# Performance work log

Measured on AMD Instinct MI355X. Metric: run time of the kernel, lower is better.

The kernel has to match this reference:

```python
import jax, jax.numpy as jnp
import numpy as np

B, L, E, H, DV, V = 256, 512, 200, 256, 30000, 50000
NEG_INF = -jnp.inf

def setup_inputs() -> dict:
    key = jax.random.key(0)
    ks = jax.random.split(key, 16)
    s = 0.05
    f = jnp.float32
    return {
        "input_id": jax.random.randint(ks[0], (B, 1), 0, V),
        "input_emb": jax.random.normal(ks[1], (B, 1, E), f),
        "encoder_outputs": jax.random.normal(ks[2], (B, L, H), f),
        "encoder_input_ids": jax.random.randint(ks[3], (B, L), 0, V),
        "hidden": jax.random.normal(ks[4], (B, 1, H), f),
        "attention": jax.random.normal(ks[5], (B, 1, H), f),
        # GRU (PyTorch layout): W_ih (3H, 2H+E), W_hh (3H, H), gate order r,z,n
        "W_ih": jax.random.normal(ks[6], (3 * H, 2 * H + E), f) * s,
        "W_hh": jax.random.normal(ks[7], (3 * H, H), f) * s,
        "b_ih": jnp.zeros((3 * H,), f),
        "b_hh": jnp.zeros((3 * H,), f),
        "W_attn": jax.random.normal(ks[8], (H, H), f) * s,
        "b_attn": jnp.zeros((H,), f),
        "W_comb": jax.random.normal(ks[9], (H, 2 * H), f) * s,
        "b_comb": jnp.zeros((H,), f),
        "W_gen": jax.random.normal(ks[10], (DV, H), f) * s,
        "b_gen": jnp.zeros((DV,), f),
        "W_copy": jax.random.normal(ks[11], (H, H), f) * s,
        "b_copy": jnp.zeros((H,), f),
    }


def reference(input_id, input_emb, encoder_outputs, encoder_input_ids, hidden,
              attention, W_ih, W_hh, b_ih, b_hh, W_attn, b_attn, W_comb,
              b_comb, W_gen, b_gen, W_copy, b_copy):
    b, l = encoder_input_ids.shape
    # selective read: rou = normalized match mask (NaN guard -> 0)
    mask = (input_id == encoder_input_ids).astype(encoder_outputs.dtype)  # (b,l)
    msum = jnp.sum(mask, axis=1, keepdims=True)
    rou = jnp.where(msum > 0, mask / jnp.where(msum > 0, msum, 1.0), 0.0)
    selective_read = jnp.einsum('bl,blh->bh', rou, encoder_outputs)  # (b,h)

    # GRU single step (dropout is identity at inference)
    x = jnp.concatenate([input_emb[:, 0], attention[:, 0], selective_read], axis=-1)
    h_prev = hidden[:, 0]  # (b,h)
    gx = x @ W_ih.T + b_ih          # (b,3h)
    gh = h_prev @ W_hh.T + b_hh     # (b,3h)
    xr, xz, xn = jnp.split(gx, 3, axis=-1)
    hr, hz, hn = jnp.split(gh, 3, axis=-1)
    r = jax.nn.sigmoid(xr + hr)
    z = jax.nn.sigmoid(xz + hz)
    n = jnp.tanh(xn + r * hn)
    h = (1.0 - z) * n + z * h_prev  # (b,h) cur_hidden

    # attention
    q = h @ W_attn.T + b_attn
    attn_w = jax.nn.softmax(jnp.einsum('bh,blh->bl', q, encoder_outputs), axis=-1)
    attn_applied = jnp.einsum('bl,blh->bh', attn_w, encoder_outputs)
    cur_attention = jnp.tanh(
        jnp.concatenate([attn_applied, h], axis=-1) @ W_comb.T + b_comb)  # (b,h)

    # generate + copy scores, joint softmax
    generate_score = cur_attention @ W_gen.T + b_gen                     # (b,DV)
    copy_weights = jax.nn.sigmoid(encoder_outputs @ W_copy.T + b_copy)   # (b,l,h)
    copy_score = jnp.einsum('blh,bh->bl', copy_weights, cur_attention)   # (b,l)
    score = jax.nn.softmax(jnp.concatenate([generate_score, copy_score], axis=1), axis=1)
    gen_s, copy_s = score[:, :DV], score[:, DV:]

    # fused equivalent of the one-hot scatter/mix: direct scatter-add into vocab
    output = jnp.zeros((b, V), score.dtype)
    output = output.at[:, :DV].add(gen_s)
    output = output.at[jnp.arange(b)[:, None], encoder_input_ids].add(copy_s)

    pos = output > 0
    out = jnp.where(pos, jnp.log(jnp.where(pos, output, 1.0)), NEG_INF)
    return out, h[:, None, :], cur_attention[:, None, :]
```

## Files before the change

### kernel.cpp

```cpp
#include <hip/hip_runtime.h>
#include <cmath>

#define B_  256
#define L_  512
#define E_  200
#define H_  256
#define DV_ 30000
#define V_  50000
#define X_  712
#define G3_ 768
#define NT_ 235

#define NEG_BIG -1.0e30f

typedef __attribute__((ext_vector_type(8))) _Float16 half8;
typedef __attribute__((ext_vector_type(4))) float   floatx4;

#define GLOAD16(gptr, lptr)                                                            \
    __builtin_amdgcn_global_load_lds(                                                  \
        (const __attribute__((address_space(1))) unsigned int*)(gptr),                 \
        (__attribute__((address_space(3))) unsigned int*)(lptr), 16, 0, 0)

__global__ void k_selread(const int* __restrict__ input_id, const float* __restrict__ emb,
                          const float* __restrict__ attention, const float* __restrict__ hidden,
                          const float* __restrict__ enc, const int* __restrict__ enc_ids,
                          const float* __restrict__ Wc, _Float16* __restrict__ wcb,
                          float* __restrict__ xT) {
    int b = blockIdx.x, t = threadIdx.x;
    __shared__ int cnt;
    __shared__ int list[L_];
    if (t == 0) cnt = 0;
    __syncthreads();
    wcb[b * H_ + t] = (_Float16)Wc[b * H_ + t];
    int id = input_id[b];
    for (int l = t; l < L_; l += 256) {
        if (enc_ids[b * L_ + l] == id) { int p = atomicAdd(&cnt, 1); list[p] = l; }
    }
    __syncthreads();
    int n = cnt;
    float s = 0.f;
    for (int i = 0; i < n; i++) s += enc[(b * L_ + list[i]) * H_ + t];
    float sel = (n > 0) ? s / (float)n : 0.f;
    for (int k = t; k < E_; k += 256) xT[k * B_ + b] = emb[b * E_ + k];
    xT[(E_ + t) * B_ + b]       = attention[b * H_ + t];
    xT[(E_ + H_ + t) * B_ + b]  = sel;
    xT[(X_ + t) * B_ + b]       = hidden[b * H_ + t];
}

template<int K, int OS>
__global__ void __launch_bounds__(256) k_gru_one(const float* __restrict__ xTp, const float* __restrict__ W,
                                                 const float* __restrict__ bias, float* __restrict__ g) {
    __shared__ __align__(16) float Ws[8 * K];
    int t  = threadIdx.x;
    int j0 = blockIdx.x * 8;
    int bq = t & 63;
    int jh = t >> 6;
#pragma unroll
    for (int jj = 0; jj < 8; jj++) {
        const float4* src = (const float4*)(W + (size_t)(j0 + jj) * K);
        float4* dst = (float4*)(Ws + jj * K);
        for (int i = t; i < K / 4; i += 256) dst[i] = src[i];
    }
    __syncthreads();
    float acc0[4] = {0.f, 0.f, 0.f, 0.f};
    float acc1[4] = {0.f, 0.f, 0.f, 0.f};
    const float* w0 = Ws + (jh * 2 + 0) * K;
    const float* w1 = Ws + (jh * 2 + 1) * K;
#pragma unroll 2
    for (int k4 = 0; k4 < K / 4; k4++) {
        float4 wa = *(const float4*)(w0 + k4 * 4);
        float4 wb = *(const float4*)(w1 + k4 * 4);
        float wav[4] = {wa.x, wa.y, wa.z, wa.w};
        float wbv[4] = {wb.x, wb.y, wb.z, wb.w};
#pragma unroll
        for (int u = 0; u < 4; u++) {
            float4 xv = *(const float4*)(xTp + (size_t)(k4 * 4 + u) * B_ + bq * 4);
            acc0[0] += wav[u] * xv.x; acc0[1] += wav[u] * xv.y;
            acc0[2] += wav[u] * xv.z; acc0[3] += wav[u] * xv.w;
            acc1[0] += wbv[u] * xv.x; acc1[1] += wbv[u] * xv.y;
            acc1[2] += wbv[u] * xv.z; acc1[3] += wbv[u] * xv.w;
        }
    }
    int ja = j0 + jh * 2, jb = ja + 1;
    float ba = bias[ja], bb = bias[jb];
#pragma unroll
    for (int i = 0; i < 4; i++) {
        g[(size_t)(bq * 4 + i) * OS + ja] = acc0[i] + ba;
        g[(size_t)(bq * 4 + i) * OS + jb] = acc1[i] + bb;
    }
}

__global__ void k_gru_gates(const float* __restrict__ gx, const float* __restrict__ gh,
                            const float* __restrict__ hidden, float* __restrict__ hws,
                            float* __restrict__ hT, float* __restrict__ hout) {
    int b = blockIdx.x, j = threadIdx.x;
    float xr = gx[b * G3_ + j], xz = gx[b * G3_ + 256 + j], xn = gx[b * G3_ + 512 + j];
    float hr = gh[b * G3_ + j], hz = gh[b * G3_ + 256 + j], hn = gh[b * G3_ + 512 + j];
    float r = 1.f / (1.f + expf(-(xr + hr)));
    float z = 1.f / (1.f + expf(-(xz + hz)));
    float n = tanhf(xn + r * hn);
    float hp = hidden[b * H_ + j];
    float h = (1.f - z) * n + z * hp;
    hws[b * H_ + j] = h;
    hT[j * B_ + b]  = h;
    hout[b * H_ + j] = h;
}

#define NC_ 4
#define CR_ 128
__global__ void __launch_bounds__(256) k_attn_a(const float* __restrict__ qws, const float* __restrict__ enc,
                         float* __restrict__ avp, float* __restrict__ mdp) {
    int blk = blockIdx.x;
    int b = blk >> 2, c = blk & 3;
    int t = threadIdx.x, lane = t & 63, w = t >> 6;
    __shared__ float ps[CR_];
    __shared__ float red[8];
    __shared__ __align__(16) float pavs[4][H_];
    const float* encc = enc + ((size_t)b * L_ + c * CR_) * H_;
    float4 q4 = *(const float4*)&qws[b * H_ + lane * 4];
    for (int i = 0; i < 32; i += 8) {
        float s[8];
#pragma unroll
        for (int u = 0; u < 8; u++) {
            float4 e = *(const float4*)(encc + (size_t)(w * 32 + i + u) * H_ + lane * 4);
            s[u] = q4.x * e.x + q4.y * e.y + q4.z * e.z + q4.w * e.w;
        }
#pragma unroll
        for (int u = 0; u < 8; u++) {
#pragma unroll
            for (int o = 1; o < 64; o <<= 1) s[u] += __shfl_xor(s[u], o);
            if (lane == 0) ps[w * 32 + i + u] = s[u];
        }
    }
    __syncthreads();
    {
        float v = ps[w * 32 + (lane & 31)];
#pragma unroll
        for (int o = 1; o < 64; o <<= 1) v = fmaxf(v, __shfl_xor(v, o));
        if (lane == 0) red[w] = v;
    }
    __syncthreads();
    float M = fmaxf(fmaxf(red[0], red[1]), fmaxf(red[2], red[3]));
    float e = (t < CR_) ? __expf(ps[t] - M) : 0.f;
    {
        float ssum = e;
#pragma unroll
        for (int o = 1; o < 64; o <<= 1) ssum += __shfl_xor(ssum, o);
        if (lane == 0) red[4 + w] = ssum;
    }
    __syncthreads();
    if (t < CR_) ps[t] = e;
    if (t == 0) {
        mdp[blk * 2]     = M;
        mdp[blk * 2 + 1] = red[4] + red[5] + red[6] + red[7];
    }
    __syncthreads();
    {
        float4 av = {0.f, 0.f, 0.f, 0.f};
        const float* encg = encc + (size_t)w * 32 * H_;
        const float* psg  = &ps[w * 32];
#pragma unroll 4
        for (int r = 0; r < 32; r++) {
            float p = psg[r];
            float4 ev = *(const float4*)(encg + (size_t)r * H_ + lane * 4);
            av.x += p * ev.x; av.y += p * ev.y; av.z += p * ev.z; av.w += p * ev.w;
        }
        *(float4*)&pavs[w][lane * 4] = av;
    }
    __syncthreads();
    avp[(size_t)blk * H_ + t] = pavs[0][t] + pavs[1][t] + pavs[2][t] + pavs[3][t];
}

__global__ void __launch_bounds__(256) k_attn_b(const float* __restrict__ avp, const float* __restrict__ mdp,
                         const float* __restrict__ hws, const float* __restrict__ W_comb,
                         const float* __restrict__ b_comb,
                         float* __restrict__ caws, _Float16* __restrict__ cab,
                         float* __restrict__ caout) {
    int b = blockIdx.x, t = threadIdx.x;
    __shared__ __align__(16) float xs[2 * H_];
    float m0 = mdp[(b * 4 + 0) * 2], d0 = mdp[(b * 4 + 0) * 2 + 1];
    float m1 = mdp[(b * 4 + 1) * 2], d1 = mdp[(b * 4 + 1) * 2 + 1];
    float m2 = mdp[(b * 4 + 2) * 2], d2 = mdp[(b * 4 + 2) * 2 + 1];
    float m3 = mdp[(b * 4 + 3) * 2], d3 = mdp[(b * 4 + 3) * 2 + 1];
    float M = fmaxf(fmaxf(m0, m1), fmaxf(m2, m3));
    float f0 = __expf(m0 - M), f1 = __expf(m1 - M), f2 = __expf(m2 - M), f3 = __expf(m3 - M);
    float den = f0 * d0 + f1 * d1 + f2 * d2 + f3 * d3;
    float num = f0 * avp[((size_t)b * 4 + 0) * H_ + t] + f1 * avp[((size_t)b * 4 + 1) * H_ + t]
              + f2 * avp[((size_t)b * 4 + 2) * H_ + t] + f3 * avp[((size_t)b * 4 + 3) * H_ + t];
    xs[t]      = num / den;
    xs[H_ + t] = hws[b * H_ + t];
    __syncthreads();
    const float4* wr = (const float4*)(W_comb + (size_t)t * (2 * H_));
    const float4* xp = (const float4*)xs;
    float acc = 0.f;
#pragma unroll 8
    for (int k4 = 0; k4 < 128; k4++) {
        float4 wv = wr[k4], xv = xp[k4];
        acc += wv.x * xv.x + wv.y * xv.y + wv.z * xv.z + wv.w * xv.w;
    }
    float cav = tanhf(b_comb[t] + acc);
    caws[b * H_ + t]  = cav;
    cab[b * H_ + t]   = (_Float16)cav;
    caout[b * H_ + t] = cav;
}

__global__ void __launch_bounds__(256, 2) k_gen_mfma(
        const _Float16* __restrict__ cab, const float* __restrict__ W_gen,
        const float* __restrict__ b_gen, float* __restrict__ out,
        float2* __restrict__ pmd) {
    __shared__ __align__(16) _Float16 Ah[128 * 32];
    __shared__ __align__(16) float    Bf[128 * 32];
    __shared__ float mm[4][128], dd[4][128];
    int t = threadIdx.x, w = t >> 6, lane = t & 63;
    int n0 = blockIdx.x * 128, m0 = blockIdx.y * 128;
    int wm = (w >> 1) * 64, wn = (w & 1) * 64;
    int l15 = lane & 15, q = lane >> 4;
    floatx4 acc[4][4];
#pragma unroll
    for (int i = 0; i < 4; i++)
#pragma unroll
        for (int j = 0; j < 4; j++) acc[i][j] = (floatx4){0.f, 0.f, 0.f, 0.f};

    for (int kc = 0; kc < H_; kc += 32) {
#pragma unroll
        for (int i = 0; i < 2; i++) {
            int t2 = w * 2 + i;
            int row = t2 * 16 + (lane >> 2);
            int sl  = (lane & 3) ^ ((row >> 1) & 3);
            const _Float16* g = cab + (size_t)(m0 + row) * H_ + kc + sl * 8;
            GLOAD16(g, &Ah[t2 * 512]);
        }
#pragma unroll
        for (int i = 0; i < 4; i++) {
            int t2 = w * 4 + i;
            int row = t2 * 8 + (lane >> 3);
            int sl  = (lane & 7) ^ (row & 7);
            int nn = n0 + row; nn = nn < DV_ ? nn : DV_ - 1;
            const float* g = W_gen + (size_t)nn * H_ + kc + sl * 4;
            GLOAD16(g, &Bf[t2 * 256]);
        }
        __syncthreads();
        half8 a[4];
#pragma unroll
        for (int mi = 0; mi < 4; mi++) {
            int m = wm + mi * 16 + l15;
            a[mi] = *(const half8*)&Ah[m * 32 + (q ^ ((m >> 1) & 3)) * 8];
        }
#pragma unroll
        for (int ni = 0; ni < 4; ni++) {
            int n = wn + ni * 16 + l15;
            const float* bb = &Bf[n * 32];
            float4 f0 = *(const float4*)&bb[((q * 2 + 0) ^ (n & 7)) * 4];
            float4 f1 = *(const float4*)&bb[((q * 2 + 1) ^ (n & 7)) * 4];
            half8 bf;
            bf[0] = (_Float16)f0.x; bf[1] = (_Float16)f0.y; bf[2] = (_Float16)f0.z; bf[3] = (_Float16)f0.w;
            bf[4] = (_Float16)f1.x; bf[5] = (_Float16)f1.y; bf[6] = (_Float16)f1.z; bf[7] = (_Float16)f1.w;
#pragma unroll
            for (int mi = 0; mi < 4; mi++)
                acc[mi][ni] = __builtin_amdgcn_mfma_f32_16x16x32_f16(a[mi], bf, acc[mi][ni], 0, 0, 0);
        }
        __syncthreads();
    }
    float bgs[4];
#pragma unroll
    for (int ni = 0; ni < 4; ni++) {
        int col = n0 + wn + ni * 16 + l15;
        if (col < DV_) {
            float bg = b_gen[col];
            bgs[ni] = bg;
#pragma unroll
            for (int mi = 0; mi < 4; mi++)
#pragma unroll
                for (int j = 0; j < 4; j++) {
                    int row = m0 + wm + mi * 16 + q * 4 + j;
                    out[(size_t)row * V_ + col] = acc[mi][ni][j] + bg;
                }
        } else bgs[ni] = 0.f;
    }
#pragma unroll
    for (int mi = 0; mi < 4; mi++)
#pragma unroll
        for (int j = 0; j < 4; j++) {
            float m_l = -INFINITY, d_l = 0.f;
#pragma unroll
            for (int ni = 0; ni < 4; ni++) {
                int col = n0 + wn + ni * 16 + l15;
                float v = (col < DV_) ? acc[mi][ni][j] + bgs[ni] : NEG_BIG;
                float mn = fmaxf(m_l, v);
                d_l = d_l * __expf(m_l - mn) + __expf(v - mn);
                m_l = mn;
            }
#pragma unroll
            for (int o = 1; o < 16; o <<= 1) {
                float m2 = __shfl_xor(m_l, o), d2 = __shfl_xor(d_l, o);
                float mn = fmaxf(m_l, m2);
                d_l = d_l * __expf(m_l - mn) + d2 * __expf(m2 - mn);
                m_l = mn;
            }
            if (l15 == 0) {
                int rl = wm + mi * 16 + q * 4 + j;
                mm[w][rl] = m_l; dd[w][rl] = d_l;
            }
        }
    __syncthreads();
    if (t < 128) {
        int wa = (t < 64) ? 0 : 2;
        float ma = mm[wa][t],     da = dd[wa][t];
        float mb = mm[wa + 1][t], db = dd[wa + 1][t];
        float M = fmaxf(ma, mb);
        float D = da * __expf(ma - M) + db * __expf(mb - M);
        pmd[(size_t)(m0 + t) * NT_ + blockIdx.x] = make_float2(M, D);
    }
}

__global__ void __launch_bounds__(256, 2) k_copy_mfma(
        const float* __restrict__ enc, const _Float16* __restrict__ wcb,
        const float* __restrict__ b_copy, const float* __restrict__ caws,
        float* __restrict__ copy_s) {
    __shared__ __align__(16) float    Af[128 * 32];
    __shared__ __align__(16) _Float16 Bh[256 * 32];
    __shared__ float bcs[H_], cas[H_];
    int t = threadIdx.x, w = t >> 6, lane = t & 63;
    int R0 = blockIdx.x * 128;
    int b  = blockIdx.x >> 2;
    int l15 = lane & 15, q = lane >> 4;
    bcs[t] = b_copy[t];
    cas[t] = caws[b * H_ + t];
    floatx4 acc[2][16];
#pragma unroll
    for (int i = 0; i < 2; i++)
#pragma unroll
        for (int j = 0; j < 16; j++) acc[i][j] = (floatx4){0.f, 0.f, 0.f, 0.f};

    for (int kc = 0; kc < H_; kc += 32) {
#pragma unroll
        for (int i = 0; i < 4; i++) {
            int t2 = w * 4 + i;
            int row = t2 * 8 + (lane >> 3);
            int sl  = (lane & 7) ^ (row & 7);
            const float* g = enc + (size_t)(R0 + row) * H_ + kc + sl * 4;
            GLOAD16(g, &Af[t2 * 256]);
        }
#pragma unroll
        for (int i = 0; i < 4; i++) {
            int t2 = w * 4 + i;
            int row = t2 * 16 + (lane >> 2);
            int sl  = (lane & 3) ^ ((row >> 1) & 3);
            const _Float16* g = wcb + row * H_ + kc + sl * 8;
            GLOAD16(g, &Bh[t2 * 512]);
        }
        __syncthreads();
        half8 a[2];
#pragma unroll
        for (int mi = 0; mi < 2; mi++) {
            int m = w * 32 + mi * 16 + l15;
            const float* ar = &Af[m * 32];
            float4 f0 = *(const float4*)&ar[((q * 2 + 0) ^ (m & 7)) * 4];
            float4 f1 = *(const float4*)&ar[((q * 2 + 1) ^ (m & 7)) * 4];
            half8 h;
            h[0] = (_Float16)f0.x; h[1] = (_Float16)f0.y; h[2] = (_Float16)f0.z; h[3] = (_Float16)f0.w;
            h[4] = (_Float16)f1.x; h[5] = (_Float16)f1.y; h[6] = (_Float16)f1.z; h[7] = (_Float16)f1.w;
            a[mi] = h;
        }
#pragma unroll
        for (int ni = 0; ni < 16; ni++) {
            int n = ni * 16 + l15;
            half8 bf = *(const half8*)&Bh[n * 32 + (q ^ ((n >> 1) & 3)) * 8];
            acc[0][ni] = __builtin_amdgcn_mfma_f32_16x16x32_f16(a[0], bf, acc[0][ni], 0, 0, 0);
            acc[1][ni] = __builtin_amdgcn_mfma_f32_16x16x32_f16(a[1], bf, acc[1][ni], 0, 0, 0);
        }
        __syncthreads();
    }
#pragma unroll
    for (int mi = 0; mi < 2; mi++) {
#pragma unroll
        for (int j = 0; j < 4; j++) {
            float p = 0.f;
#pragma unroll
            for (int ni = 0; ni < 16; ni++) {
                int col = ni * 16 + l15;
                float v = acc[mi][ni][j] + bcs[col];
                p += cas[col] / (1.f + __expf(-v));
            }
            p += __shfl_xor(p, 1);
            p += __shfl_xor(p, 2);
            p += __shfl_xor(p, 4);
            p += __shfl_xor(p, 8);
            if (l15 == 0) copy_s[R0 + w * 32 + mi * 16 + q * 4 + j] = p;
        }
    }
}

__global__ void __launch_bounds__(256) k_stats2(const float2* __restrict__ pmd, const float* __restrict__ copy_s,
                         float* __restrict__ mrow, float* __restrict__ ldrow) {
    int b = blockIdx.x, t = threadIdx.x, lane = t & 63, w = t >> 6;
    __shared__ float rm[4], rs[4];
    float m = -INFINITY, d = 0.f;
    if (t < NT_) { float2 p = pmd[(size_t)b * NT_ + t]; m = p.x; d = p.y; }
    float v0 = copy_s[b * L_ + t];
    float v1 = copy_s[b * L_ + 256 + t];
    float mn = fmaxf(m, v0); d = d * __expf(m - mn) + __expf(v0 - mn); m = mn;
    mn = fmaxf(m, v1); d = d * __expf(m - mn) + __expf(v1 - mn); m = mn;
#pragma unroll
    for (int o = 1; o < 64; o <<= 1) {
        float m2 = __shfl_xor(m, o), d2 = __shfl_xor(d, o);
        mn = fmaxf(m, m2);
        d = d * __expf(m - mn) + d2 * __expf(m2 - mn);
        m = mn;
    }
    if (lane == 0) { rm[w] = m; rs[w] = d; }
    __syncthreads();
    if (t == 0) {
        float M = rm[0], S = rs[0];
        for (int i = 1; i < 4; i++) {
            float mx = fmaxf(M, rm[i]);
            S = S * __expf(M - mx) + rs[i] * __expf(rm[i] - mx);
            M = mx;
        }
        mrow[b] = M;
        ldrow[b] = __logf(S);
    }
}

__global__ void __launch_bounds__(256) k_final(float* __restrict__ out, const float* __restrict__ mrow,
                        const float* __restrict__ ldrow) {
    int idx = blockIdx.x * 256 + threadIdx.x;
    int b = blockIdx.y;
    if (idx >= V_ / 4) return;
    float4* o4 = (float4*)(out + (size_t)b * V_) + idx;
    if (idx >= DV_ / 4) {
        *o4 = make_float4(NEG_BIG, NEG_BIG, NEG_BIG, NEG_BIG);
        return;
    }
    float sh = mrow[b] + ldrow[b];
    float4 v = *o4;
    v.x -= sh; v.y -= sh; v.z -= sh; v.w -= sh;
    *o4 = v;
}

__global__ void k_scatter_log(float* __restrict__ out, const float* __restrict__ copy_s,
                              const int* __restrict__ enc_ids, const float* __restrict__ mrow,
                              const float* __restrict__ ldrow) {
    int l = blockIdx.x * 256 + threadIdx.x;
    int b = blockIdx.y;
    float p = __expf(copy_s[b * L_ + l] - mrow[b] - ldrow[b]);
    unsigned int* up = (unsigned int*)(out + (size_t)b * V_ + enc_ids[b * L_ + l]);
    unsigned int cur = *up;
    while (true) {
        float ov = __uint_as_float(cur);
        float pv = (ov < -1.0e29f) ? p : __expf(ov) + p;
        unsigned int prev = atomicCAS(up, cur, __float_as_uint(__logf(pv)));
        if (prev == cur) break;
        cur = prev;
    }
}

extern "C" void kernel_launch(void* const* d_in, const int* in_sizes, int n_in,
                              void* d_out, int out_size, void* d_ws, size_t ws_size,
                              hipStream_t stream) {
    const int*   input_id  = (const int*)  d_in[0];
    const float* input_emb = (const float*)d_in[1];
    const float* enc       = (const float*)d_in[2];
    const int*   enc_ids   = (const int*)  d_in[3];
    const float* hidden    = (const float*)d_in[4];
    const float* attention = (const float*)d_in[5];
    const float* W_ih      = (const float*)d_in[6];
    const float* W_hh      = (const float*)d_in[7];
    const float* b_ih      = (const float*)d_in[8];
    const float* b_hh      = (const float*)d_in[9];
    const float* W_attn    = (const float*)d_in[10];
    const float* b_attn    = (const float*)d_in[11];
    const float* W_comb    = (const float*)d_in[12];
    const float* b_comb    = (const float*)d_in[13];
    const float* W_gen     = (const float*)d_in[14];
    const float* b_gen     = (const float*)d_in[15];
    const float* W_copy    = (const float*)d_in[16];
    const float* b_copy    = (const float*)d_in[17];

    float* out = (float*)d_out;
    float* ws  = (float*)d_ws;
    float* xT   = ws;
    float* gx   = xT + 247808;
    float* gh   = gx + 196608;
    float* hws  = gh + 196608;
    float* caws = hws + 65536;
    float* cps  = caws + 65536;
    float* mrow = cps + 131072;
    float* ldrow = mrow + 256;
    _Float16* wcb = (_Float16*)(ldrow + 256);
    _Float16* cab = wcb + 65536;
    float* qws  = (float*)(cab + 65536);
    float* mdp  = qws + 65536;
    float2* pmd = (float2*)(mdp + 2048);
    float* hT   = xT;
    float* avp  = gx;

    float* hout  = out + (size_t)B_ * V_;
    float* caout = hout + B_ * H_;

    k_selread<<<256, 256, 0, stream>>>(input_id, input_emb, attention, hidden, enc, enc_ids, W_copy, wcb, xT);
    k_gru_one<712, G3_><<<96, 256, 0, stream>>>(xT, W_ih, b_ih, gx);
    k_gru_one<256, G3_><<<96, 256, 0, stream>>>(xT + X_ * B_, W_hh, b_hh, gh);
    k_gru_gates<<<256, 256, 0, stream>>>(gx, gh, hidden, hws, hT, hout);
    k_gru_one<256, H_><<<32, 256, 0, stream>>>(hT, W_attn, b_attn, qws);
    k_attn_a<<<B_ * NC_, 256, 0, stream>>>(qws, enc, avp, mdp);
    k_attn_b<<<256, 256, 0, stream>>>(avp, mdp, hws, W_comb, b_comb, caws, cab, caout);
    k_gen_mfma<<<dim3(NT_, 2), 256, 0, stream>>>(cab, W_gen, b_gen, out, pmd);
    k_copy_mfma<<<(B_ * L_) / 128, 256, 0, stream>>>(enc, wcb, b_copy, caws, cps);
    k_stats2<<<256, 256, 0, stream>>>(pmd, cps, mrow, ldrow);
    dim3 gf((V_ / 4 + 255) / 256, B_);
    k_final<<<gf, 256, 0, stream>>>(out, mrow, ldrow);
    dim3 gs(L_ / 256, B_);
    k_scatter_log<<<gs, 256, 0, stream>>>(out, cps, enc_ids, mrow, ldrow);
}
```

Baseline: 447.6 us.

## Merge generate and copy GEMMs into one launch with double-buffered LDS staging

```diff
diff --git a/kernel.cpp b/kernel.cpp
--- a/kernel.cpp
+++ b/kernel.cpp
@@ -10,6 +10,8 @@
 #define X_  712
 #define G3_ 768
 #define NT_ 235
+#define NBC_ 1024
+#define NBG_ 470
 
 #define NEG_BIG -1.0e30f
 
@@ -204,189 +206,209 @@
     caout[b * H_ + t] = cav;
 }
 
-__global__ void __launch_bounds__(256, 2) k_gen_mfma(
+__global__ void __launch_bounds__(256, 2) k_gc(
+        const float* __restrict__ enc, const _Float16* __restrict__ wcb,
+        const float* __restrict__ b_copy, const float* __restrict__ caws,
+        float* __restrict__ copy_s,
         const _Float16* __restrict__ cab, const float* __restrict__ W_gen,
         const float* __restrict__ b_gen, float* __restrict__ out,
         float2* __restrict__ pmd) {
-    __shared__ __align__(16) _Float16 Ah[128 * 32];
-    __shared__ __align__(16) float    Bf[128 * 32];
-    __shared__ float mm[4][128], dd[4][128];
+    __shared__ __align__(16) unsigned char smem[67584];
     int t = threadIdx.x, w = t >> 6, lane = t & 63;
-    int n0 = blockIdx.x * 128, m0 = blockIdx.y * 128;
-    int wm = (w >> 1) * 64, wn = (w & 1) * 64;
     int l15 = lane & 15, q = lane >> 4;
-    floatx4 acc[4][4];
-#pragma unroll
-    for (int i = 0; i < 4; i++)
-#pragma unroll
-        for (int j = 0; j < 4; j++) acc[i][j] = (floatx4){0.f, 0.f, 0.f, 0.f};
-
-    for (int kc = 0; kc < H_; kc += 32) {
-#pragma unroll
-        for (int i = 0; i < 2; i++) {
-            int t2 = w * 2 + i;
-            int row = t2 * 16 + (lane >> 2);
-            int sl  = (lane & 3) ^ ((row >> 1) & 3);
-            const _Float16* g = cab + (size_t)(m0 + row) * H_ + kc + sl * 8;
-            GLOAD16(g, &Ah[t2 * 512]);
-        }
-#pragma unroll
-        for (int i = 0; i < 4; i++) {
-            int t2 = w * 4 + i;
-            int row = t2 * 8 + (lane >> 3);
-            int sl  = (lane & 7) ^ (row & 7);
-            int nn = n0 + row; nn = nn < DV_ ? nn : DV_ - 1;
-            const float* g = W_gen + (size_t)nn * H_ + kc + sl * 4;
-            GLOAD16(g, &Bf[t2 * 256]);
-        }
+
+    if (blockIdx.x < NBC_) {
+        float*    Af = (float*)smem;
+        _Float16* Bh = (_Float16*)(smem + 32768);
+        float*    bcs = (float*)(smem + 65536);
+        float*    cas = bcs + H_;
+        int cb = blockIdx.x;
+        int R0 = cb * 128;
+        int b  = cb >> 2;
+        bcs[t] = b_copy[t];
+        cas[t] = caws[b * H_ + t];
+        floatx4 acc[2][16];
+#pragma unroll
+        for (int i = 0; i < 2; i++)
+#pragma unroll
+            for (int j = 0; j < 16; j++) acc[i][j] = (floatx4){0.f, 0.f, 0.f, 0.f};
+
+#define STAGE_CPY(KC, BUF)                                                              \
+        {                                                                               \
+            _Pragma("unroll")                                                           \
+            for (int i = 0; i < 4; i++) {                                               \
+                int t2 = w * 4 + i;                                                     \
+                int row = t2 * 8 + (lane >> 3);                                         \
+                int sl  = (lane & 7) ^ (row & 7);                                       \
+                GLOAD16(enc + (size_t)(R0 + row) * H_ + (KC) + sl * 4,                  \
+                        &Af[(BUF) * 4096 + t2 * 256]);                                  \
+            }                                                                           \
+            _Pragma("unroll")                                                           \
+            for (int i = 0; i < 4; i++) {                                               \
+                int t2 = w * 4 + i;                                                     \
+                int row = t2 * 16 + (lane >> 2);                                        \
+                int sl  = (lane & 3) ^ ((row >> 1) & 3);                                \
+                GLOAD16(wcb + row * H_ + (KC) + sl * 8,                                 \
+                        &Bh[(BUF) * 8192 + t2 * 512]);                                  \
+            }                                                                           \
+        }
+        STAGE_CPY(0, 0);
         __syncthreads();
-        half8 a[4];
-#pragma unroll
-        for (int mi = 0; mi < 4; mi++) {
-            int m = wm + mi * 16 + l15;
-            a[mi] = *(const half8*)&Ah[m * 32 + (q ^ ((m >> 1) & 3)) * 8];
-        }
+        int cur = 0;
+        for (int kc8 = 0; kc8 < 8; kc8++) {
+            if (kc8 < 7) STAGE_CPY((kc8 + 1) * 32, cur ^ 1);
+            half8 a[2];
+#pragma unroll
+            for (int mi = 0; mi < 2; mi++) {
+                int m = w * 32 + mi * 16 + l15;
+                const float* ar = &Af[cur * 4096 + m * 32];
+                float4 f0 = *(const float4*)&ar[((q * 2 + 0) ^ (m & 7)) * 4];
+                float4 f1 = *(const float4*)&ar[((q * 2 + 1) ^ (m & 7)) * 4];
+                half8 h;
+                h[0] = (_Float16)f0.x; h[1] = (_Float16)f0.y; h[2] = (_Float16)f0.z; h[3] = (_Float16)f0.w;
+                h[4] = (_Float16)f1.x; h[5] = (_Float16)f1.y; h[6] = (_Float16)f1.z; h[7] = (_Float16)f1.w;
+                a[mi] = h;
+            }
+#pragma unroll
+            for (int ni = 0; ni < 16; ni++) {
+                int n = ni * 16 + l15;
+                half8 bf = *(const half8*)&Bh[cur * 8192 + n * 32 + (q ^ ((n >> 1) & 3)) * 8];
+                acc[0][ni] = __builtin_amdgcn_mfma_f32_16x16x32_f16(a[0], bf, acc[0][ni], 0, 0, 0);
+                acc[1][ni] = __builtin_amdgcn_mfma_f32_16x16x32_f16(a[1], bf, acc[1][ni], 0, 0, 0);
+            }
+            __syncthreads();
+            cur ^= 1;
+        }
+#pragma unroll
+        for (int mi = 0; mi < 2; mi++) {
+#pragma unroll
+            for (int j = 0; j < 4; j++) {
+                float p = 0.f;
+#pragma unroll
+                for (int ni = 0; ni < 16; ni++) {
+                    int col = ni * 16 + l15;
+                    float v = acc[mi][ni][j] + bcs[col];
+                    p += cas[col] / (1.f + __expf(-v));
+                }
+                p += __shfl_xor(p, 1);
+                p += __shfl_xor(p, 2);
+                p += __shfl_xor(p, 4);
+                p += __shfl_xor(p, 8);
+                if (l15 == 0) copy_s[R0 + w * 32 + mi * 16 + q * 4 + j] = p;
+            }
+        }
+    } else {
+        _Float16* Ah = (_Float16*)smem;
+        float*    Bf = (float*)(smem + 16384);
+        float*    mm = (float*)(smem + 49152);
+        float*    dd = mm + 512;
+        int g  = blockIdx.x - NBC_;
+        int bx = (g < NT_) ? g : g - NT_;
+        int by = (g < NT_) ? 0 : 1;
+        int n0 = bx * 128, m0 = by * 128;
+        int wm = (w >> 1) * 64, wn = (w & 1) * 64;
+        floatx4 acc[4][4];
+#pragma unroll
+        for (int i = 0; i < 4; i++)
+#pragma unroll
+            for (int j = 0; j < 4; j++) acc[i][j] = (floatx4){0.f, 0.f, 0.f, 0.f};
+
+#define STAGE_GEN(KC, BUF)                                                              \
+        {                                                                               \
+            _Pragma("unroll")                                                           \
+            for (int i = 0; i < 2; i++) {                                               \
+                int t2 = w * 2 + i;                                                     \
+                int row = t2 * 16 + (lane >> 2);                                        \
+                int sl  = (lane & 3) ^ ((row >> 1) & 3);                                \
+                GLOAD16(cab + (size_t)(m0 + row) * H_ + (KC) + sl * 8,                  \
+                        &Ah[(BUF) * 4096 + t2 * 512]);                                  \
+            }                                                                           \
+            _Pragma("unroll")                                                           \
+            for (int i = 0; i < 4; i++) {                                               \
+                int t2 = w * 4 + i;                                                     \
+                int row = t2 * 8 + (lane >> 3);                                         \
+                int sl  = (lane & 7) ^ (row & 7);                                       \
+                int nn = n0 + row; nn = nn < DV_ ? nn : DV_ - 1;                        \
+                GLOAD16(W_gen + (size_t)nn * H_ + (KC) + sl * 4,                        \
+                        &Bf[(BUF) * 4096 + t2 * 256]);                                  \
+            }                                                                           \
+        }
+        STAGE_GEN(0, 0);
+        __syncthreads();
+        int cur = 0;
+        for (int kc8 = 0; kc8 < 8; kc8++) {
+            if (kc8 < 7) STAGE_GEN((kc8 + 1) * 32, cur ^ 1);
+            half8 a[4];
+#pragma unroll
+            for (int mi = 0; mi < 4; mi++) {
+                int m = wm + mi * 16 + l15;
+                a[mi] = *(const half8*)&Ah[cur * 4096 + m * 32 + (q ^ ((m >> 1) & 3)) * 8];
+            }
+#pragma unroll
+            for (int ni = 0; ni < 4; ni++) {
+                int n = wn + ni * 16 + l15;
+                const float* bb = &Bf[cur * 4096 + n * 32];
+                float4 f0 = *(const float4*)&bb[((q * 2 + 0) ^ (n & 7)) * 4];
+                float4 f1 = *(const float4*)&bb[((q * 2 + 1) ^ (n & 7)) * 4];
+                half8 bf;
+                bf[0] = (_Float16)f0.x; bf[1] = (_Float16)f0.y; bf[2] = (_Float16)f0.z; bf[3] = (_Float16)f0.w;
+                bf[4] = (_Float16)f1.x; bf[5] = (_Float16)f1.y; bf[6] = (_Float16)f1.z; bf[7] = (_Float16)f1.w;
+#pragma unroll
+                for (int mi = 0; mi < 4; mi++)
+                    acc[mi][ni] = __builtin_amdgcn_mfma_f32_16x16x32_f16(a[mi], bf, acc[mi][ni], 0, 0, 0);
+            }
+            __syncthreads();
+            cur ^= 1;
+        }
+        float bgs[4];
 #pragma unroll
         for (int ni = 0; ni < 4; ni++) {
-            int n = wn + ni * 16 + l15;
-            const float* bb = &Bf[n * 32];
-            float4 f0 = *(const float4*)&bb[((q * 2 + 0) ^ (n & 7)) * 4];
-            float4 f1 = *(const float4*)&bb[((q * 2 + 1) ^ (n & 7)) * 4];
-            half8 bf;
-            bf[0] = (_Float16)f0.x; bf[1] = (_Float16)f0.y; bf[2] = (_Float16)f0.z; bf[3] = (_Float16)f0.w;
-            bf[4] = (_Float16)f1.x; bf[5] = (_Float16)f1.y; bf[6] = (_Float16)f1.z; bf[7] = (_Float16)f1.w;
-#pragma unroll
-            for (int mi = 0; mi < 4; mi++)
-                acc[mi][ni] = __builtin_amdgcn_mfma_f32_16x16x32_f16(a[mi], bf, acc[mi][ni], 0, 0, 0);
-        }
+            int col = n0 + wn + ni * 16 + l15;
+            if (col < DV_) {
+                float bg = b_gen[col];
+                bgs[ni] = bg;
+#pragma unroll
+                for (int mi = 0; mi < 4; mi++)
+#pragma unroll
+                    for (int j = 0; j < 4; j++) {
+                        int row = m0 + wm + mi * 16 + q * 4 + j;
+                        out[(size_t)row * V_ + col] = acc[mi][ni][j] + bg;
+                    }
+            } else bgs[ni] = 0.f;
+        }
+#pragma unroll
+        for (int mi = 0; mi < 4; mi++)
+#pragma unroll
+            for (int j = 0; j < 4; j++) {
+                float m_l = -INFINITY, d_l = 0.f;
+#pragma unroll
+                for (int ni = 0; ni < 4; ni++) {
+                    int col = n0 + wn + ni * 16 + l15;
+                    float v = (col < DV_) ? acc[mi][ni][j] + bgs[ni] : NEG_BIG;
+                    float mn = fmaxf(m_l, v);
+                    d_l = d_l * __expf(m_l - mn) + __expf(v - mn);
+                    m_l = mn;
+                }
+#pragma unroll
+                for (int o = 1; o < 16; o <<= 1) {
+                    float m2 = __shfl_xor(m_l, o), d2 = __shfl_xor(d_l, o);
+                    float mn = fmaxf(m_l, m2);
+                    d_l = d_l * __expf(m_l - mn) + d2 * __expf(m2 - mn);
+                    m_l = mn;
+                }
+                if (l15 == 0) {
+                    int rl = wm + mi * 16 + q * 4 + j;
+                    mm[w * 128 + rl] = m_l; dd[w * 128 + rl] = d_l;
+                }
+            }
         __syncthreads();
-    }
-    float bgs[4];
-#pragma unroll
-    for (int ni = 0; ni < 4; ni++) {
-        int col = n0 + wn + ni * 16 + l15;
-        if (col < DV_) {
-            float bg = b_gen[col];
-            bgs[ni] = bg;
-#pragma unroll
-            for (int mi = 0; mi < 4; mi++)
-#pragma unroll
-                for (int j = 0; j < 4; j++) {
-                    int row = m0 + wm + mi * 16 + q * 4 + j;
-                    out[(size_t)row * V_ + col] = acc[mi][ni][j] + bg;
-                }
-        } else bgs[ni] = 0.f;
-    }
-#pragma unroll
-    for (int mi = 0; mi < 4; mi++)
-#pragma unroll
-        for (int j = 0; j < 4; j++) {
-            float m_l = -INFINITY, d_l = 0.f;
-#pragma unroll
-            for (int ni = 0; ni < 4; ni++) {
-                int col = n0 + wn + ni * 16 + l15;
-                float v = (col < DV_) ? acc[mi][ni][j] + bgs[ni] : NEG_BIG;
-                float mn = fmaxf(m_l, v);
-                d_l = d_l * __expf(m_l - mn) + __expf(v - mn);
-                m_l = mn;
-            }
-#pragma unroll
-            for (int o = 1; o < 16; o <<= 1) {
-                float m2 = __shfl_xor(m_l, o), d2 = __shfl_xor(d_l, o);
-                float mn = fmaxf(m_l, m2);
-                d_l = d_l * __expf(m_l - mn) + d2 * __expf(m2 - mn);
-                m_l = mn;
-            }
-            if (l15 == 0) {
-                int rl = wm + mi * 16 + q * 4 + j;
-                mm[w][rl] = m_l; dd[w][rl] = d_l;
-            }
-        }
-    __syncthreads();
-    if (t < 128) {
-        int wa = (t < 64) ? 0 : 2;
-        float ma = mm[wa][t],     da = dd[wa][t];
-        float mb = mm[wa + 1][t], db = dd[wa + 1][t];
-        float M = fmaxf(ma, mb);
-        float D = da * __expf(ma - M) + db * __expf(mb - M);
-        pmd[(size_t)(m0 + t) * NT_ + blockIdx.x] = make_float2(M, D);
-    }
-}
-
-__global__ void __launch_bounds__(256, 2) k_copy_mfma(
-        const float* __restrict__ enc, const _Float16* __restrict__ wcb,
-        const float* __restrict__ b_copy, const float* __restrict__ caws,
-        float* __restrict__ copy_s) {
-    __shared__ __align__(16) float    Af[128 * 32];
-    __shared__ __align__(16) _Float16 Bh[256 * 32];
-    __shared__ float bcs[H_], cas[H_];
-    int t = threadIdx.x, w = t >> 6, lane = t & 63;
-    int R0 = blockIdx.x * 128;
-    int b  = blockIdx.x >> 2;
-    int l15 = lane & 15, q = lane >> 4;
-    bcs[t] = b_copy[t];
-    cas[t] = caws[b * H_ + t];
-    floatx4 acc[2][16];
-#pragma unroll
-    for (int i = 0; i < 2; i++)
-#pragma unroll
-        for (int j = 0; j < 16; j++) acc[i][j] = (floatx4){0.f, 0.f, 0.f, 0.f};
-
-    for (int kc = 0; kc < H_; kc += 32) {
-#pragma unroll
-        for (int i = 0; i < 4; i++) {
-            int t2 = w * 4 + i;
-            int row = t2 * 8 + (lane >> 3);
-            int sl  = (lane & 7) ^ (row & 7);
-            const float* g = enc + (size_t)(R0 + row) * H_ + kc + sl * 4;
-            GLOAD16(g, &Af[t2 * 256]);
-        }
-#pragma unroll
-        for (int i = 0; i < 4; i++) {
-            int t2 = w * 4 + i;
-            int row = t2 * 16 + (lane >> 2);
-            int sl  = (lane & 3) ^ ((row >> 1) & 3);
-            const _Float16* g = wcb + row * H_ + kc + sl * 8;
-            GLOAD16(g, &Bh[t2 * 512]);
-        }
-        __syncthreads();
-        half8 a[2];
-#pragma unroll
-        for (int mi = 0; mi < 2; mi++) {
-            int m = w * 32 + mi * 16 + l15;
-            const float* ar = &Af[m * 32];
-            float4 f0 = *(const float4*)&ar[((q * 2 + 0) ^ (m & 7)) * 4];
-            float4 f1 = *(const float4*)&ar[((q * 2 + 1) ^ (m & 7)) * 4];
-            half8 h;
-            h[0] = (_Float16)f0.x; h[1] = (_Float16)f0.y; h[2] = (_Float16)f0.z; h[3] = (_Float16)f0.w;
-            h[4] = (_Float16)f1.x; h[5] = (_Float16)f1.y; h[6] = (_Float16)f1.z; h[7] = (_Float16)f1.w;
-            a[mi] = h;
-        }
-#pragma unroll
-        for (int ni = 0; ni < 16; ni++) {
-            int n = ni * 16 + l15;
-            half8 bf = *(const half8*)&Bh[n * 32 + (q ^ ((n >> 1) & 3)) * 8];
-            acc[0][ni] = __builtin_amdgcn_mfma_f32_16x16x32_f16(a[0], bf, acc[0][ni], 0, 0, 0);
-            acc[1][ni] = __builtin_amdgcn_mfma_f32_16x16x32_f16(a[1], bf, acc[1][ni], 0, 0, 0);
-        }
-        __syncthreads();
-    }
-#pragma unroll
-    for (int mi = 0; mi < 2; mi++) {
-#pragma unroll
-        for (int j = 0; j < 4; j++) {
-            float p = 0.f;
-#pragma unroll
-            for (int ni = 0; ni < 16; ni++) {
-                int col = ni * 16 + l15;
-                float v = acc[mi][ni][j] + bcs[col];
-                p += cas[col] / (1.f + __expf(-v));
-            }
-            p += __shfl_xor(p, 1);
-            p += __shfl_xor(p, 2);
-            p += __shfl_xor(p, 4);
-            p += __shfl_xor(p, 8);
-            if (l15 == 0) copy_s[R0 + w * 32 + mi * 16 + q * 4 + j] = p;
+        if (t < 128) {
+            int wa = (t < 64) ? 0 : 2;
+            float ma = mm[wa * 128 + t],       da = dd[wa * 128 + t];
+            float mb = mm[(wa + 1) * 128 + t], db = dd[(wa + 1) * 128 + t];
+            float M = fmaxf(ma, mb);
+            float D = da * __expf(ma - M) + db * __expf(mb - M);
+            pmd[(size_t)(m0 + t) * NT_ + bx] = make_float2(M, D);
         }
     }
 }
@@ -505,8 +527,7 @@
     k_gru_one<256, H_><<<32, 256, 0, stream>>>(hT, W_attn, b_attn, qws);
     k_attn_a<<<B_ * NC_, 256, 0, stream>>>(qws, enc, avp, mdp);
     k_attn_b<<<256, 256, 0, stream>>>(avp, mdp, hws, W_comb, b_comb, caws, cab, caout);
-    k_gen_mfma<<<dim3(NT_, 2), 256, 0, stream>>>(cab, W_gen, b_gen, out, pmd);
-    k_copy_mfma<<<(B_ * L_) / 128, 256, 0, stream>>>(enc, wcb, b_copy, caws, cps);
+    k_gc<<<NBC_ + NBG_, 256, 0, stream>>>(enc, wcb, b_copy, caws, cps, cab, W_gen, b_gen, out, pmd);
     k_stats2<<<256, 256, 0, stream>>>(pmd, cps, mrow, ldrow);
     dim3 gf((V_ / 4 + 255) / 256, B_);
     k_final<<<gf, 256, 0, stream>>>(out, mrow, ldrow);
```

Result: no change. 444.9 us (-0.6%).
